# Kernel optimization log

Hardware: AMD Instinct MI355X
Metric: run time of the kernel (lower is better)

Reference implementation:

```python
import jax, jax.numpy as jnp
import numpy as np

B, N, C, K = 2048, 64, 256, 3  # batch, num_proposals, hidden_dim, kernel_size
EPS = 1e-5


def setup_inputs() -> dict:
    key = jax.random.key(0)
    k0, k1, k2 = jax.random.split(key, 3)
    query = jax.random.normal(k0, (B, N, C), dtype=jnp.float32)
    value = jax.random.normal(k1, (B, N, C), dtype=jnp.float32)
    # weight_linear: Linear(C, N + K), trunc_normal std=0.02, zero bias
    W_lin = (jax.random.truncated_normal(k2, -2.0, 2.0, (N + K, C), dtype=jnp.float32) * 0.02)
    b_lin = jnp.zeros((N + K,), dtype=jnp.float32)
    ln_gamma = jnp.ones((C,), dtype=jnp.float32)
    ln_beta = jnp.zeros((C,), dtype=jnp.float32)
    return {"query": query, "value": value, "W_lin": W_lin, "b_lin": b_lin,
            "ln_gamma": ln_gamma, "ln_beta": ln_beta}


def reference(query, value, W_lin, b_lin, ln_gamma, ln_beta):
    # dynamic weights: [B, N, N + K]
    dyw = jnp.einsum('bnc,oc->bno', query, W_lin) + b_lin
    depth_w = dyw[..., :K]          # [B, N, K]  per-proposal depthwise kernel
    point_w = dyw[..., K:]          # [B, M, N]  out-proposal m mixes in-proposal n

    # depthwise conv1d over C with padding='same' (torch conv1d = cross-correlation)
    vpad = jnp.pad(value, ((0, 0), (0, 0), (1, 1)))                 # [B, N, C+2]
    win = jnp.stack([vpad[..., k:k + C] for k in range(K)], axis=2)  # [B, N, K, C]
    depth = jax.nn.relu(jnp.einsum('bnkc,bnk->bnc', win, depth_w))   # [B, N, C]

    # pointwise (1x1) conv mixing the N proposal channels
    point = jnp.einsum('bmn,bnc->bmc', point_w, depth)               # [B, N, C]

    # LayerNorm over last dim C
    mu = jnp.mean(point, axis=-1, keepdims=True)
    var = jnp.mean(jnp.square(point - mu), axis=-1, keepdims=True)
    out = (point - mu) * jax.lax.rsqrt(var + EPS) * ln_gamma + ln_beta
    return out
```

## Files before the change

### kernel.cpp

```cpp
#include <hip/hip_runtime.h>

#define NB 2048
#define NN 64
#define NC 256
#define EPSV 1e-5f

typedef __attribute__((ext_vector_type(8))) short bf16x8;
typedef __attribute__((ext_vector_type(4))) float f32x4;

union U8 { unsigned u[4]; unsigned long long d[2]; bf16x8 v; };

__device__ __forceinline__ unsigned f_bits(float f) {
    union { float f; unsigned u; } x; x.f = f; return x.u;
}
__device__ __forceinline__ unsigned short f2bf_r(float f) {
    return (unsigned short)((f_bits(f) + 0x8000u) >> 16);
}
__device__ __forceinline__ unsigned pack2(float a, float b) {
    return ((f_bits(a) + 0x8000u) >> 16) | ((f_bits(b) + 0x8000u) & 0xffff0000u);
}

extern "C" __global__ void prep_wfrag(const float* __restrict__ W,
                                      unsigned short* __restrict__ wf)
{
    const int idx = blockIdx.x * 256 + threadIdx.x;
    if (idx >= 40 * 64) return;
    const int f = idx >> 6, l = idx & 63;
    const int nt = f >> 3, kg = f & 7;
    const int o = nt * 16 + (l & 15);
    const int kb = kg * 32 + (l >> 4) * 8;
    float x[8];
#pragma unroll
    for (int e = 0; e < 8; ++e)
        x[e] = (o < 67) ? W[o * NC + kb + e] : 0.f;
    uint4 pk;
    pk.x = pack2(x[0], x[1]); pk.y = pack2(x[2], x[3]);
    pk.z = pack2(x[4], x[5]); pk.w = pack2(x[6], x[7]);
    *(uint4*)(wf + (size_t)idx * 8) = pk;
}

extern "C" __global__ __launch_bounds__(512, 6)
void dysep_mfma8(const float* __restrict__ q, const float* __restrict__ v,
                 const unsigned short* __restrict__ wfrag,
                 const float* __restrict__ bl,
                 const float* __restrict__ gam, const float* __restrict__ bet,
                 float* __restrict__ out)
{
    __shared__ __align__(16) unsigned short sDT[256 * 66];
    __shared__ __align__(16) unsigned short sPw[64][68];
    __shared__ __align__(16) float sCw[64][4];
    __shared__ __align__(16) float sLN[64][4];

    const int tid = threadIdx.x;
    const int w  = tid >> 6;
    const int mt = w & 3;
    const int h  = w >> 2;
    const int l  = tid & 63;
    const int lr = l & 15;
    const int lg = l >> 4;
    const long base = (long)blockIdx.x * (NN * NC);

    bf16x8 af[8];
    {
        const float* qrow = q + base + (long)(mt * 16 + lr) * NC + lg * 8;
#pragma unroll
        for (int kg = 0; kg < 8; ++kg) {
            float4 a0 = *(const float4*)(qrow + kg * 32);
            float4 a1 = *(const float4*)(qrow + kg * 32 + 4);
            U8 u;
            u.u[0] = pack2(a0.x, a0.y); u.u[1] = pack2(a0.z, a0.w);
            u.u[2] = pack2(a1.x, a1.y); u.u[3] = pack2(a1.z, a1.w);
            af[kg] = u.v;
        }
    }
    const int ntCount = 3 - h;
    f32x4 acc[3];
    {
        f32x4 zz = {0.f, 0.f, 0.f, 0.f};
#pragma unroll
        for (int t = 0; t < 3; ++t) acc[t] = zz;
    }
    const U8* __restrict__ wf8 = (const U8*)wfrag;
#pragma unroll
    for (int t = 0; t < 3; ++t) {
        if (t < ntCount) {
            const int nt = h * 3 + t;
            const U8* fr = wf8 + (nt * 8) * 64 + l;
#pragma unroll
            for (int kg = 0; kg < 8; ++kg) {
                U8 u = fr[kg * 64];
                acc[t] = __builtin_amdgcn_mfma_f32_16x16x32_bf16(af[kg], u.v, acc[t], 0, 0, 0);
            }
        }
    }
#pragma unroll
    for (int t = 0; t < 3; ++t) {
        if (t < ntCount) {
            const int o = (h * 3 + t) * 16 + lr;
            const float bb = (o < 67) ? bl[o] : 0.f;
#pragma unroll
            for (int r = 0; r < 4; ++r) {
                const int m = mt * 16 + lg * 4 + r;
                const float val = acc[t][r] + bb;
                if (o < 3) sCw[m][o] = val;
                else if (o < 67) sPw[m][o - 3] = f2bf_r(val);
            }
        }
    }
    __syncthreads();

    {
#pragma unroll 4
        for (int i = 0; i < 8; ++i) {
            const int n = i * 8 + w;
            const float w0 = sCw[n][0], w1 = sCw[n][1], w2 = sCw[n][2];
            float4 vv = *(const float4*)(v + base + (long)n * NC + 4 * l);
            float prev = __shfl(vv.w, (l + 63) & 63);
            float next = __shfl(vv.x, (l + 1) & 63);
            if (l == 0) prev = 0.f;
            if (l == 63) next = 0.f;
            const float d0 = fmaxf(0.f, w0 * prev + w1 * vv.x + w2 * vv.y);
            const float d1 = fmaxf(0.f, w0 * vv.x + w1 * vv.y + w2 * vv.z);
            const float d2 = fmaxf(0.f, w0 * vv.y + w1 * vv.z + w2 * vv.w);
            const float d3 = fmaxf(0.f, w0 * vv.z + w1 * vv.w + w2 * next);
            const int c0 = 4 * l;
            sDT[(c0 + 0) * 66 + n] = f2bf_r(d0);
            sDT[(c0 + 1) * 66 + n] = f2bf_r(d1);
            sDT[(c0 + 2) * 66 + n] = f2bf_r(d2);
            sDT[(c0 + 3) * 66 + n] = f2bf_r(d3);
        }
    }
    __syncthreads();

    bf16x8 pa[2];
#pragma unroll
    for (int kg = 0; kg < 2; ++kg) {
        const unsigned long long* p =
            (const unsigned long long*)&sPw[mt * 16 + lr][kg * 32 + lg * 8];
        U8 u; u.d[0] = p[0]; u.d[1] = p[1];
        pa[kg] = u.v;
    }
    f32x4 acc3[8];
    {
        f32x4 zz = {0.f, 0.f, 0.f, 0.f};
#pragma unroll
        for (int t = 0; t < 8; ++t) acc3[t] = zz;
    }
#pragma unroll
    for (int t = 0; t < 8; ++t) {
        const int ct = h * 8 + t;
#pragma unroll
        for (int kg = 0; kg < 2; ++kg) {
            const unsigned* p = (const unsigned*)&sDT[(ct * 16 + lr) * 66 + kg * 32 + lg * 8];
            U8 u; u.u[0] = p[0]; u.u[1] = p[1]; u.u[2] = p[2]; u.u[3] = p[3];
            acc3[t] = __builtin_amdgcn_mfma_f32_16x16x32_bf16(pa[kg], u.v, acc3[t], 0, 0, 0);
        }
    }
    {
        float s1a[4], s2a[4];
#pragma unroll
        for (int r = 0; r < 4; ++r) {
            float s1 = 0.f, s2 = 0.f;
#pragma unroll
            for (int t = 0; t < 8; ++t) {
                const float x = acc3[t][r];
                s1 += x; s2 += x * x;
            }
#pragma unroll
            for (int off = 1; off < 16; off <<= 1) {
                s1 += __shfl_xor(s1, off);
                s2 += __shfl_xor(s2, off);
            }
            s1a[r] = s1; s2a[r] = s2;
        }
        if (lr == 0) {
#pragma unroll
            for (int r = 0; r < 4; ++r) {
                const int m = mt * 16 + lg * 4 + r;
                sLN[m][2 * h + 0] = s1a[r];
                sLN[m][2 * h + 1] = s2a[r];
            }
        }
    }
    __syncthreads();

    float mus[4], rss[4];
#pragma unroll
    for (int r = 0; r < 4; ++r) {
        const int m = mt * 16 + lg * 4 + r;
        const float S1 = sLN[m][0] + sLN[m][2];
        const float S2 = sLN[m][1] + sLN[m][3];
        const float mu = S1 * (1.f / 256.f);
        const float var = S2 * (1.f / 256.f) - mu * mu;
        mus[r] = mu;
        rss[r] = rsqrtf(var + EPSV);
    }
    {
        float* orow = out + base + (long)(mt * 16 + lg * 4) * NC + lr;
#pragma unroll
        for (int t = 0; t < 8; ++t) {
            const int ct = h * 8 + t;
            const float gg = gam[ct * 16 + lr];
            const float bb = bet[ct * 16 + lr];
#pragma unroll
            for (int r = 0; r < 4; ++r) {
                orow[(long)r * NC + ct * 16] =
                    (acc3[t][r] - mus[r]) * rss[r] * gg + bb;
            }
        }
    }
}

extern "C" void kernel_launch(void* const* d_in, const int* in_sizes, int n_in,
                              void* d_out, int out_size, void* d_ws, size_t ws_size,
                              hipStream_t stream) {
    const float* q   = (const float*)d_in[0];
    const float* v   = (const float*)d_in[1];
    const float* W   = (const float*)d_in[2];
    const float* bl  = (const float*)d_in[3];
    const float* gam = (const float*)d_in[4];
    const float* bet = (const float*)d_in[5];
    float* o = (float*)d_out;
    unsigned short* wf = (unsigned short*)d_ws;

    hipLaunchKernelGGL(prep_wfrag, dim3(10), dim3(256), 0, stream, W, wf);
    hipLaunchKernelGGL(dysep_mfma8, dim3(NB), dim3(512), 0, stream,
                       q, v, wf, bl, gam, bet, o);
}
```

Before: 109.3 us.

## Split fused kernel into dynamic-weight GEMM kernel and conv+mix+LayerNorm kernel

After: 119.6 us. +9.4%, slower.

```diff
diff --git a/kernel.cpp b/kernel.cpp
--- a/kernel.cpp
+++ b/kernel.cpp
@@ -37,6 +37,189 @@
     pk.x = pack2(x[0], x[1]); pk.y = pack2(x[2], x[3]);
     pk.z = pack2(x[4], x[5]); pk.w = pack2(x[6], x[7]);
     *(uint4*)(wf + (size_t)idx * 8) = pk;
+}
+
+extern "C" __global__ __launch_bounds__(512)
+void dysep_k1(const float* __restrict__ q, const unsigned short* __restrict__ wfrag,
+              const float* __restrict__ bl,
+              float* __restrict__ cw_out, unsigned short* __restrict__ pw_out)
+{
+    const int tid = threadIdx.x;
+    const int w  = tid >> 6;
+    const int mt = w & 3;
+    const int h  = w >> 2;
+    const int l  = tid & 63;
+    const int lr = l & 15;
+    const int lg = l >> 4;
+    const int b  = blockIdx.x;
+    const long base = (long)b * (NN * NC);
+
+    bf16x8 af[8];
+    {
+        const float* qrow = q + base + (long)(mt * 16 + lr) * NC + lg * 8;
+#pragma unroll
+        for (int kg = 0; kg < 8; ++kg) {
+            float4 a0 = *(const float4*)(qrow + kg * 32);
+            float4 a1 = *(const float4*)(qrow + kg * 32 + 4);
+            U8 u;
+            u.u[0] = pack2(a0.x, a0.y); u.u[1] = pack2(a0.z, a0.w);
+            u.u[2] = pack2(a1.x, a1.y); u.u[3] = pack2(a1.z, a1.w);
+            af[kg] = u.v;
+        }
+    }
+    const int ntCount = 3 - h;
+    f32x4 acc[3];
+    {
+        f32x4 zz = {0.f, 0.f, 0.f, 0.f};
+#pragma unroll
+        for (int t = 0; t < 3; ++t) acc[t] = zz;
+    }
+    const U8* __restrict__ wf8 = (const U8*)wfrag;
+#pragma unroll
+    for (int t = 0; t < 3; ++t) {
+        if (t < ntCount) {
+            const int nt = h * 3 + t;
+            const U8* fr = wf8 + (nt * 8) * 64 + l;
+#pragma unroll
+            for (int kg = 0; kg < 8; ++kg) {
+                U8 u = fr[kg * 64];
+                acc[t] = __builtin_amdgcn_mfma_f32_16x16x32_bf16(af[kg], u.v, acc[t], 0, 0, 0);
+            }
+        }
+    }
+#pragma unroll
+    for (int t = 0; t < 3; ++t) {
+        if (t < ntCount) {
+            const int o = (h * 3 + t) * 16 + lr;
+            const float bb = (o < 67) ? bl[o] : 0.f;
+#pragma unroll
+            for (int r = 0; r < 4; ++r) {
+                const int m = mt * 16 + lg * 4 + r;
+                const float val = acc[t][r] + bb;
+                if (o < 3) cw_out[b * 256 + m * 4 + o] = val;
+                else if (o < 67) pw_out[(size_t)b * 4096 + m * 64 + (o - 3)] = f2bf_r(val);
+            }
+        }
+    }
+}
+
+extern "C" __global__ __launch_bounds__(512, 6)
+void dysep_k2(const float* __restrict__ v, const float* __restrict__ cw_in,
+              const unsigned short* __restrict__ pw_in,
+              const float* __restrict__ gam, const float* __restrict__ bet,
+              float* __restrict__ out)
+{
+    __shared__ __align__(16) unsigned short sDT[256 * 66];
+    __shared__ __align__(16) float sLN[64][4];
+
+    const int tid = threadIdx.x;
+    const int w  = tid >> 6;
+    const int mt = w & 3;
+    const int h  = w >> 2;
+    const int l  = tid & 63;
+    const int lr = l & 15;
+    const int lg = l >> 4;
+    const int b  = blockIdx.x;
+    const long base = (long)b * (NN * NC);
+
+#pragma unroll
+    for (int i = 0; i < 8; ++i) {
+        const int n = i * 8 + w;
+        float4 vv  = *(const float4*)(v + base + (long)n * NC + 4 * l);
+        float4 cwv = *(const float4*)(cw_in + b * 256 + n * 4);
+        float prev = __shfl(vv.w, (l + 63) & 63);
+        float next = __shfl(vv.x, (l + 1) & 63);
+        if (l == 0) prev = 0.f;
+        if (l == 63) next = 0.f;
+        const float d0 = fmaxf(0.f, cwv.x * prev + cwv.y * vv.x + cwv.z * vv.y);
+        const float d1 = fmaxf(0.f, cwv.x * vv.x + cwv.y * vv.y + cwv.z * vv.z);
+        const float d2 = fmaxf(0.f, cwv.x * vv.y + cwv.y * vv.z + cwv.z * vv.w);
+        const float d3 = fmaxf(0.f, cwv.x * vv.z + cwv.y * vv.w + cwv.z * next);
+        const int c0 = 4 * l;
+        sDT[(c0 + 0) * 66 + n] = f2bf_r(d0);
+        sDT[(c0 + 1) * 66 + n] = f2bf_r(d1);
+        sDT[(c0 + 2) * 66 + n] = f2bf_r(d2);
+        sDT[(c0 + 3) * 66 + n] = f2bf_r(d3);
+    }
+    __syncthreads();
+
+    bf16x8 pa[2];
+#pragma unroll
+    for (int kg = 0; kg < 2; ++kg) {
+        const unsigned long long* p = (const unsigned long long*)
+            (pw_in + (size_t)b * 4096 + (mt * 16 + lr) * 64 + kg * 32 + lg * 8);
+        U8 u; u.d[0] = p[0]; u.d[1] = p[1];
+        pa[kg] = u.v;
+    }
+    f32x4 acc3[8];
+    {
+        f32x4 zz = {0.f, 0.f, 0.f, 0.f};
+#pragma unroll
+        for (int t = 0; t < 8; ++t) acc3[t] = zz;
+    }
+#pragma unroll
+    for (int t = 0; t < 8; ++t) {
+        const int ct = h * 8 + t;
+#pragma unroll
+        for (int kg = 0; kg < 2; ++kg) {
+            const unsigned* p = (const unsigned*)&sDT[(ct * 16 + lr) * 66 + kg * 32 + lg * 8];
+            U8 u; u.u[0] = p[0]; u.u[1] = p[1]; u.u[2] = p[2]; u.u[3] = p[3];
+            acc3[t] = __builtin_amdgcn_mfma_f32_16x16x32_bf16(pa[kg], u.v, acc3[t], 0, 0, 0);
+        }
+    }
+    {
+        float s1a[4], s2a[4];
+#pragma unroll
+        for (int r = 0; r < 4; ++r) {
+            float s1 = 0.f, s2 = 0.f;
+#pragma unroll
+            for (int t = 0; t < 8; ++t) {
+                const float x = acc3[t][r];
+                s1 += x; s2 += x * x;
+            }
+#pragma unroll
+            for (int off = 1; off < 16; off <<= 1) {
+                s1 += __shfl_xor(s1, off);
+                s2 += __shfl_xor(s2, off);
+            }
+            s1a[r] = s1; s2a[r] = s2;
+        }
+        if (lr == 0) {
+#pragma unroll
+            for (int r = 0; r < 4; ++r) {
+                const int m = mt * 16 + lg * 4 + r;
+                sLN[m][2 * h + 0] = s1a[r];
+                sLN[m][2 * h + 1] = s2a[r];
+            }
+        }
+    }
+    __syncthreads();
+
+    float mus[4], rss[4];
+#pragma unroll
+    for (int r = 0; r < 4; ++r) {
+        const int m = mt * 16 + lg * 4 + r;
+        const float S1 = sLN[m][0] + sLN[m][2];
+        const float S2 = sLN[m][1] + sLN[m][3];
+        const float mu = S1 * (1.f / 256.f);
+        const float var = S2 * (1.f / 256.f) - mu * mu;
+        mus[r] = mu;
+        rss[r] = rsqrtf(var + EPSV);
+    }
+    {
+        float* orow = out + base + (long)(mt * 16 + lg * 4) * NC + lr;
+#pragma unroll
+        for (int t = 0; t < 8; ++t) {
+            const int ct = h * 8 + t;
+            const float gg = gam[ct * 16 + lr];
+            const float bb = bet[ct * 16 + lr];
+#pragma unroll
+            for (int r = 0; r < 4; ++r) {
+                orow[(long)r * NC + ct * 16] =
+                    (acc3[t][r] - mus[r]) * rss[r] * gg + bb;
+            }
+        }
+    }
 }
 
 extern "C" __global__ __launch_bounds__(512, 6)
@@ -221,9 +404,26 @@
     const float* gam = (const float*)d_in[4];
     const float* bet = (const float*)d_in[5];
     float* o = (float*)d_out;
+
+    const size_t WF_SZ  = 40960;
+    const size_t CW_OFF = WF_SZ;
+    const size_t CW_SZ  = (size_t)NB * 64 * 4 * 4;
+    const size_t PW_OFF = CW_OFF + CW_SZ;
+    const size_t PW_SZ  = (size_t)NB * 64 * 64 * 2;
+    const size_t NEED   = PW_OFF + PW_SZ;
+
     unsigned short* wf = (unsigned short*)d_ws;
-
     hipLaunchKernelGGL(prep_wfrag, dim3(10), dim3(256), 0, stream, W, wf);
-    hipLaunchKernelGGL(dysep_mfma8, dim3(NB), dim3(512), 0, stream,
-                       q, v, wf, bl, gam, bet, o);
-}
+
+    if (ws_size >= NEED) {
+        float* cw          = (float*)((char*)d_ws + CW_OFF);
+        unsigned short* pw = (unsigned short*)((char*)d_ws + PW_OFF);
+        hipLaunchKernelGGL(dysep_k1, dim3(NB), dim3(512), 0, stream,
+                           q, wf, bl, cw, pw);
+        hipLaunchKernelGGL(dysep_k2, dim3(NB), dim3(512), 0, stream,
+                           v, cw, pw, gam, bet, o);
+    } else {
+        hipLaunchKernelGGL(dysep_mfma8, dim3(NB), dim3(512), 0, stream,
+                           q, v, wf, bl, gam, bet, o);
+    }
+}
```
